# Kernel optimization log

Hardware: AMD Instinct MI355X
Metric: run time of the kernel (lower is better)

The kernel has to match this reference:

```python
import jax, jax.numpy as jnp
import numpy as np

DICT = 32768
TOP_K = 128
LN_EPS = 1e-5


def setup_inputs() -> dict:
    key = jax.random.key(0)
    k_x, k_we, k_be, k_wd, k_bd = jax.random.split(key, 5)
    B, S, D = 4, 2048, 768
    x = jax.random.normal(k_x, (B, S, D), dtype=jnp.float32)
    # nn.Linear stores weight as [out, in]; init scaled roughly like orthogonal gains
    W_enc = jax.random.normal(k_we, (DICT, D), dtype=jnp.float32) / np.sqrt(D)
    b_enc = jax.random.normal(k_be, (DICT,), dtype=jnp.float32) * 0.01
    W_dec = jax.random.normal(k_wd, (D, DICT), dtype=jnp.float32) * (0.1 / np.sqrt(DICT))
    b_dec = jax.random.normal(k_bd, (D,), dtype=jnp.float32) * 0.01
    ln_gamma = jnp.ones((DICT,), dtype=jnp.float32)
    ln_beta = jnp.zeros((DICT,), dtype=jnp.float32)
    return {"x": x, "W_enc": W_enc, "b_enc": b_enc, "ln_gamma": ln_gamma,
            "ln_beta": ln_beta, "W_dec": W_dec, "b_dec": b_dec}


def _layernorm(z, gamma, beta):
    mu = jnp.mean(z, axis=-1, keepdims=True)
    var = jnp.mean(jnp.square(z - mu), axis=-1, keepdims=True)
    return (z - mu) * jax.lax.rsqrt(var + LN_EPS) * gamma + beta


def _top_k_activation(z, k):
    # keep top-k values per row, zero elsewhere (scatter, like torch.scatter_)
    vals, idx = jax.lax.top_k(z, k)            # [B,S,k]
    out = jnp.zeros_like(z)
    return jnp.put_along_axis(out, idx, vals, axis=-1, inplace=False)


def reference(x, W_enc, b_enc, ln_gamma, ln_beta, W_dec, b_dec):
    # encoder: [B,S,D] @ [D,DICT] -> [B,S,DICT]
    z = jnp.einsum("bsd,fd->bsf", x, W_enc) + b_enc
    z = _layernorm(z, ln_gamma, ln_beta)
    z = jax.nn.relu(z)
    features = _top_k_activation(z, TOP_K)      # [B,S,DICT], mostly zero
    output = jnp.einsum("bsf,df->bsd", features, W_dec) + b_dec  # [B,S,D]
    return (output, features)
```

## Files before the change

kernel.cpp:

```cpp
#include <hip/hip_runtime.h>
#include <hip/hip_bf16.h>

#define R_TOT  8192
#define DIM    768
#define FDICT  32768
#define TOPK   128
#define LN_EPS 1e-5f
#define BAND_M 0.12f
#define BAND_CAP 192

using f32x4  = __attribute__((ext_vector_type(4))) float;
using short8 = __attribute__((ext_vector_type(8))) short;

__device__ inline short f2bf(float f) {
    __hip_bfloat16 h = __float2bfloat16(f);
    return *reinterpret_cast<short*>(&h);
}
__device__ inline float bf2f(short s) {
    return __uint_as_float(((unsigned)(unsigned short)s) << 16);
}
__device__ inline void load_lds16(const void* g, void* l) {
    __builtin_amdgcn_global_load_lds(
        (const __attribute__((address_space(1))) unsigned int*)g,
        (__attribute__((address_space(3))) unsigned int*)l, 16, 0, 0);
}

__global__ __launch_bounds__(256) void conv_bf16(
    const float* __restrict__ in, unsigned short* __restrict__ out, int n8)
{
    const int i0 = blockIdx.x * 256 + threadIdx.x;
    const int stride = gridDim.x * 256;
    for (int g = i0; g < n8; g += stride) {
        const float4 a = ((const float4*)in)[g * 2];
        const float4 b = ((const float4*)in)[g * 2 + 1];
        short8 v;
        v[0] = f2bf(a.x); v[1] = f2bf(a.y); v[2] = f2bf(a.z); v[3] = f2bf(a.w);
        v[4] = f2bf(b.x); v[5] = f2bf(b.y); v[6] = f2bf(b.z); v[7] = f2bf(b.w);
        ((short8*)out)[g] = v;
    }
}

#define READ_A(P)                                                              \
    af00 = *(const short8*)&Sb[abase + (2*(P))*1024 + sw0];                    \
    af01 = *(const short8*)&Sb[abase + (2*(P))*1024 + sw1];                    \
    af10 = *(const short8*)&Sb[abase + (2*(P)+1)*1024 + sw0];                  \
    af11 = *(const short8*)&Sb[abase + (2*(P)+1)*1024 + sw1];

#define DO_MFMA(P)                                                             \
    __builtin_amdgcn_s_setprio(1);                                             \
    _Pragma("unroll")                                                          \
    for (int n = 0; n < 4; ++n) {                                              \
        acc[2*(P)][n]   = __builtin_amdgcn_mfma_f32_16x16x32_bf16(af00, bf0[n], acc[2*(P)][n],   0,0,0); \
        acc[2*(P)][n]   = __builtin_amdgcn_mfma_f32_16x16x32_bf16(af01, bf1[n], acc[2*(P)][n],   0,0,0); \
        acc[2*(P)+1][n] = __builtin_amdgcn_mfma_f32_16x16x32_bf16(af10, bf0[n], acc[2*(P)+1][n], 0,0,0); \
        acc[2*(P)+1][n] = __builtin_amdgcn_mfma_f32_16x16x32_bf16(af11, bf1[n], acc[2*(P)+1][n], 0,0,0); \
    }                                                                          \
    __builtin_amdgcn_s_setprio(0);

__global__ __launch_bounds__(512, 2) void enc_gemm(
    const unsigned short* __restrict__ Xb, const unsigned short* __restrict__ Wb,
    const float* __restrict__ benc, unsigned short* __restrict__ Zb)
{
    __shared__ __align__(16) unsigned short S[65536];

    const int t = threadIdx.x;
    const int w = t >> 6, l = t & 63;

    const int cpx = (int)gridDim.x >> 3;
    const int swz = ((int)blockIdx.x & 7) * cpx + ((int)blockIdx.x >> 3);
    const long bm = (long)(swz >> 7) * 256;
    const long bn = (long)(swz & 127) * 256;

    const int wm = w >> 2, wn = w & 3;
    const int lrow = l & 15, l4 = l >> 4;

    const int sw0 = ((l4     ) ^ (lrow & 7)) * 8;
    const int sw1 = ((4 + l4 ) ^ (lrow & 7)) * 8;
    const int abase = wm * 8192 + lrow * 64;
    const int bbase = 16384 + wn * 4096 + lrow * 64;

    const int rh0 = w * 16 + (l >> 3);
    const int rh1 = rh0 + 8;
    const int gsl = ((l & 7) ^ (l >> 3)) * 8;
    const unsigned short* pA00 = Xb + (bm +       rh0) * DIM + gsl;
    const unsigned short* pA01 = Xb + (bm +       rh1) * DIM + gsl;
    const unsigned short* pA10 = Xb + (bm + 128 + rh0) * DIM + gsl;
    const unsigned short* pA11 = Xb + (bm + 128 + rh1) * DIM + gsl;
    const unsigned short* pB00 = Wb + (bn +       rh0) * DIM + gsl;
    const unsigned short* pB01 = Wb + (bn +       rh1) * DIM + gsl;
    const unsigned short* pB10 = Wb + (bn + 128 + rh0) * DIM + gsl;
    const unsigned short* pB11 = Wb + (bn + 128 + rh1) * DIM + gsl;
    const int d00 = w * 1024;
    const int d01 = w * 1024 + 512;

    f32x4 acc[8][4];
#pragma unroll
    for (int m = 0; m < 8; ++m)
#pragma unroll
        for (int n = 0; n < 4; ++n) acc[m][n] = (f32x4){0.f, 0.f, 0.f, 0.f};

    load_lds16(pA00, S + d00);
    load_lds16(pA01, S + d01);
    load_lds16(pA10, S + 8192 + d00);
    load_lds16(pA11, S + 8192 + d01);
    load_lds16(pB00, S + 16384 + d00);
    load_lds16(pB01, S + 16384 + d01);
    load_lds16(pB10, S + 16384 + 8192 + d00);
    load_lds16(pB11, S + 16384 + 8192 + d01);
    pA00 += 64; pA01 += 64; pA10 += 64; pA11 += 64;
    pB00 += 64; pB01 += 64; pB10 += 64; pB11 += 64;

    short8 bf0[4], bf1[4];
    short8 af00, af01, af10, af11;

#pragma unroll 1
    for (int kt = 0; kt < 12; ++kt) {
        const unsigned short* Sb = S + (kt & 1) * 32768;
        unsigned short*       Sn = S + ((kt & 1) ^ 1) * 32768;

        if (kt < 11) {
            load_lds16(pA00, Sn + d00);
            load_lds16(pA01, Sn + d01);
            load_lds16(pA10, Sn + 8192 + d00);
            load_lds16(pA11, Sn + 8192 + d01);
            asm volatile("s_waitcnt vmcnt(4)" ::: "memory");
        } else {
            asm volatile("s_waitcnt vmcnt(0)" ::: "memory");
        }
        __builtin_amdgcn_s_barrier();
#pragma unroll
        for (int n = 0; n < 4; ++n) {
            bf0[n] = *(const short8*)&Sb[bbase + n * 1024 + sw0];
            bf1[n] = *(const short8*)&Sb[bbase + n * 1024 + sw1];
        }
        READ_A(0)
        DO_MFMA(0)
        asm volatile("" ::: "memory");
        __builtin_amdgcn_s_barrier();

        READ_A(1)
        if (kt < 11) {
            load_lds16(pB00, Sn + 16384 + d00);
            load_lds16(pB01, Sn + 16384 + d01);
            load_lds16(pB10, Sn + 16384 + 8192 + d00);
            load_lds16(pB11, Sn + 16384 + 8192 + d01);
        }
        asm volatile("" ::: "memory");
        __builtin_amdgcn_s_barrier();
        DO_MFMA(1)
        asm volatile("" ::: "memory");
        __builtin_amdgcn_s_barrier();

        READ_A(2)
        asm volatile("" ::: "memory");
        __builtin_amdgcn_s_barrier();
        DO_MFMA(2)
        asm volatile("" ::: "memory");
        __builtin_amdgcn_s_barrier();

        READ_A(3)
        asm volatile("" ::: "memory");
        __builtin_amdgcn_s_barrier();
        DO_MFMA(3)
        asm volatile("" ::: "memory");
        __builtin_amdgcn_s_barrier();

        pA00 += 64; pA01 += 64; pA10 += 64; pA11 += 64;
        pB00 += 64; pB01 += 64; pB10 += 64; pB11 += 64;
    }

    __syncthreads();
    float bias[4];
#pragma unroll
    for (int n = 0; n < 4; ++n) bias[n] = benc[bn + wn * 64 + n * 16 + lrow];
    unsigned short* Cs = S;
#pragma unroll
    for (int m = 0; m < 8; ++m)
#pragma unroll
        for (int n = 0; n < 4; ++n)
#pragma unroll
            for (int q = 0; q < 4; ++q)
                Cs[(wm * 128 + m * 16 + l4 * 4 + q) * 256 + wn * 64 + n * 16 + lrow] =
                    (unsigned short)f2bf(acc[m][n][q] + bias[n]);
    __syncthreads();
#pragma unroll
    for (int it = 0; it < 16; ++it) {
        const int g = t + it * 512;
        const int row = g >> 5;
        const int c8 = (g & 31) * 8;
        const short8 v = *(const short8*)&Cs[row * 256 + c8];
        __builtin_nontemporal_store(v, (short8*)&Zb[(bm + row) * FDICT + bn + c8]);
    }
}

__global__ __launch_bounds__(1024) void topk_select(
    const unsigned short* __restrict__ Zb, const float* __restrict__ gamma,
    const float* __restrict__ beta, int* __restrict__ sel_idx,
    float* __restrict__ sel_val, int* __restrict__ band_idx,
    int* __restrict__ cdef, int* __restrict__ nband,
    float* __restrict__ muarr, float* __restrict__ sinvarr)
{
    __shared__ float    redf[32];
    __shared__ int      redi[16];
    __shared__ float    sf[3];
    __shared__ int      stot;
    __shared__ unsigned scomp[2];

    const int t = threadIdx.x;
    const int w = t >> 6;
    const long r = blockIdx.x;

    unsigned u[32];
    float sum = 0.f, sumsq = 0.f;
    const short8* Z8 = (const short8*)(Zb + r * (size_t)FDICT);
#pragma unroll
    for (int q = 0; q < 4; ++q) {
        const short8 v = Z8[q * 1024 + t];
#pragma unroll
        for (int j = 0; j < 8; ++j) {
            const float f = bf2f(v[j]);
            u[q * 8 + j] = __float_as_uint(f);
            sum += f; sumsq += f * f;
        }
    }
#pragma unroll
    for (int o = 32; o > 0; o >>= 1) {
        sum   += __shfl_down(sum, o, 64);
        sumsq += __shfl_down(sumsq, o, 64);
    }
    if ((t & 63) == 0) { redf[w] = sum; redf[16 + w] = sumsq; }
    __syncthreads();
    if (t == 0) {
        float s = 0.f, sq = 0.f;
        for (int i = 0; i < 16; ++i) { s += redf[i]; sq += redf[16 + i]; }
        const float mu = s / (float)FDICT;
        float var = sq / (float)FDICT - mu * mu;
        if (var < 0.f) var = 0.f;
        sf[0] = mu; sf[1] = 1.f / sqrtf(var + LN_EPS);
        scomp[0] = 0; scomp[1] = 0;
    }
    __syncthreads();
    const float mu = sf[0], sinv = sf[1];

    float vmax = 0.f;
#pragma unroll
    for (int q = 0; q < 4; ++q) {
        const size_t base = (size_t)(q * 1024 + t) * 8;
        const float4 g0 = *(const float4*)(gamma + base);
        const float4 g1 = *(const float4*)(gamma + base + 4);
        const float4 b0 = *(const float4*)(beta + base);
        const float4 b1 = *(const float4*)(beta + base + 4);
        const float gs[8] = {g0.x, g0.y, g0.z, g0.w, g1.x, g1.y, g1.z, g1.w};
        const float bs[8] = {b0.x, b0.y, b0.z, b0.w, b1.x, b1.y, b1.z, b1.w};
#pragma unroll
        for (int j = 0; j < 8; ++j) {
            const int i = q * 8 + j;
            const float a = fmaxf(
                fmaf((__uint_as_float(u[i]) - mu) * sinv, gs[j], bs[j]), 0.f);
            u[i] = __float_as_uint(a);
            vmax = fmaxf(vmax, a);
        }
    }
#pragma unroll
    for (int o = 32; o > 0; o >>= 1) vmax = fmaxf(vmax, __shfl_down(vmax, o, 64));
    if ((t & 63) == 0) redf[w] = vmax;
    __syncthreads();
    if (t == 0) {
        float m = 0.f;
        for (int i = 0; i < 16; ++i) m = fmaxf(m, redf[i]);
        sf[2] = m;
    }
    __syncthreads();

    float lo = 0.f, hi = sf[2] + 1e-6f;
#pragma unroll 1
    for (int it = 0; it < 9; ++it) {
        const float thr = 0.5f * (lo + hi);
        int cnt = 0;
#pragma unroll
        for (int i = 0; i < 32; ++i) cnt += (__uint_as_float(u[i]) > thr);
#pragma unroll
        for (int o = 32; o > 0; o >>= 1) cnt += __shfl_down(cnt, o, 64);
        if ((t & 63) == 0) redi[w] = cnt;
        __syncthreads();
        if (t == 0) {
            int s = 0;
            for (int i = 0; i < 16; ++i) s += redi[i];
            stot = s;
        }
        __syncthreads();
        if (stot >= TOPK) lo = thr; else hi = thr;
    }
    const float Tf = 0.5f * (lo + hi);
    const float thi = Tf + BAND_M, tlo = Tf - BAND_M;

#pragma unroll
    for (int i = 0; i < 32; ++i) {
        const float a = __uint_as_float(u[i]);
        const int idx = ((i >> 3) * 1024 + t) * 8 + (i & 7);
        if (a > thi) {
            const unsigned s = atomicAdd(&scomp[0], 1u);
            sel_idx[r * TOPK + s] = idx;
            sel_val[r * TOPK + s] = a;
        } else if (a >= tlo) {
            const unsigned s = atomicAdd(&scomp[1], 1u);
            if (s < BAND_CAP) band_idx[r * BAND_CAP + s] = idx;
        }
    }
    __syncthreads();
    if (t == 0) {
        cdef[r]  = (int)scomp[0];
        int nb = (int)scomp[1]; if (nb > BAND_CAP) nb = BAND_CAP;
        nband[r] = nb;
        muarr[r] = mu; sinvarr[r] = sinv;
    }
}

__global__ __launch_bounds__(256) void refine_select(
    const float* __restrict__ X, const float* __restrict__ Wenc,
    const float* __restrict__ benc, const float* __restrict__ gamma,
    const float* __restrict__ beta, const int* __restrict__ band_idx,
    const int* __restrict__ cdef, const int* __restrict__ nband,
    const float* __restrict__ muarr, const float* __restrict__ sinvarr,
    int* __restrict__ sel_idx, float* __restrict__ sel_val)
{
    __shared__ float xs[DIM];
    __shared__ float cval[BAND_CAP];
    __shared__ int   cidx[BAND_CAP];
    __shared__ int   scnt;
    const int t = threadIdx.x;
    const long r = blockIdx.x;
    const int w = t >> 6, l = t & 63;

    for (int i = t; i < DIM; i += 256) xs[i] = X[r * DIM + i];
    if (t == 0) scnt = 0;
    const int nb = nband[r];
    const int cd = cdef[r];
    int need = TOPK - cd; if (need > nb) need = nb;
    const double mu = (double)muarr[r], sinv = (double)sinvarr[r];
    __syncthreads();

    for (int c = w; c < nb; c += 4) {
        const int fi = band_idx[r * BAND_CAP + c];
        const float* wr = Wenc + (size_t)fi * DIM;
        double s = 0.0;
        for (int k = l; k < DIM; k += 64) s = fma((double)xs[k], (double)wr[k], s);
#pragma unroll
        for (int o = 32; o > 0; o >>= 1) s += __shfl_down(s, o, 64);
        if (l == 0) {
            const double z = s + (double)benc[fi];
            const double a = (z - mu) * sinv * (double)gamma[fi] + (double)beta[fi];
            cval[c] = fmaxf((float)a, 0.f);
            cidx[c] = fi;
        }
    }
    __syncthreads();
    if (t < nb) {
        const float v = cval[t];
        const int id = cidx[t];
        int rank = 0;
        for (int j = 0; j < nb; ++j) {
            const float vj = cval[j];
            rank += (vj > v) || (vj == v && cidx[j] < id);
        }
        if (rank < need) {
            const int s = atomicAdd(&scnt, 1);
            sel_idx[r * TOPK + cd + s] = id;
            sel_val[r * TOPK + cd + s] = v;
        }
    }
}

__global__ __launch_bounds__(256) void transposeWd(
    const float* __restrict__ Wd, unsigned short* __restrict__ WdTb)
{
    __shared__ float tile[32][33];
    const int fx = blockIdx.x * 32;
    const int dy = blockIdx.y * 32;
    const int tx = threadIdx.x & 31;
    const int ty = threadIdx.x >> 5;
    for (int i = ty; i < 32; i += 8)
        tile[i][tx] = Wd[(size_t)(dy + i) * FDICT + fx + tx];
    __syncthreads();
    for (int i = ty; i < 32; i += 8)
        WdTb[(size_t)(fx + i) * DIM + dy + tx] = (unsigned short)f2bf(tile[tx][i]);
}

__global__ __launch_bounds__(384) void decode(
    const int* __restrict__ sel_idx, const float* __restrict__ sel_val,
    const unsigned short* __restrict__ WdTb, const float* __restrict__ bdec,
    float* __restrict__ out)
{
    __shared__ int   sidx[TOPK];
    __shared__ float sval[TOPK];
    const int t = threadIdx.x;
    const long r = blockIdx.x;
    if (t < TOPK) { sidx[t] = sel_idx[r * TOPK + t]; sval[t] = sel_val[r * TOPK + t]; }
    __syncthreads();
    const float2 b2 = *(const float2*)(bdec + t * 2);
    float a0 = b2.x, a1 = b2.y;
    for (int j = 0; j < TOPK; ++j) {
        const unsigned wp = *(const unsigned*)(WdTb + (size_t)sidx[j] * DIM + t * 2);
        const float v = sval[j];
        a0 = fmaf(v, __uint_as_float((wp & 0xFFFFu) << 16), a0);
        a1 = fmaf(v, __uint_as_float(wp & 0xFFFF0000u), a1);
    }
    float2 o2; o2.x = a0; o2.y = a1;
    *(float2*)(out + r * DIM + t * 2) = o2;
}

__global__ __launch_bounds__(1024) void featfill(
    const int* __restrict__ sel_idx, const float* __restrict__ sel_val,
    float* __restrict__ feat)
{
    const int t = threadIdx.x;
    const long r = blockIdx.x;
    const f32x4 z4 = (f32x4){0.f, 0.f, 0.f, 0.f};
    f32x4* row4 = (f32x4*)(feat + r * FDICT);
    for (int i = t; i < FDICT / 4; i += 1024)
        __builtin_nontemporal_store(z4, &row4[i]);
    __syncthreads();
    if (t < TOPK)
        feat[r * FDICT + sel_idx[r * TOPK + t]] = sel_val[r * TOPK + t];
}

extern "C" void kernel_launch(void* const* d_in, const int* in_sizes, int n_in,
                              void* d_out, int out_size, void* d_ws, size_t ws_size,
                              hipStream_t stream)
{
    const float* x     = (const float*)d_in[0];
    const float* Wenc  = (const float*)d_in[1];
    const float* benc  = (const float*)d_in[2];
    const float* gamma = (const float*)d_in[3];
    const float* beta  = (const float*)d_in[4];
    const float* Wdec  = (const float*)d_in[5];
    const float* bdec  = (const float*)d_in[6];

    float* out  = (float*)d_out;
    float* feat = out + (size_t)R_TOT * DIM;

    unsigned short* Xb   = (unsigned short*)out;
    unsigned short* Zb   = (unsigned short*)feat;
    unsigned short* Wb   = (unsigned short*)((char*)feat + 536870912ull);
    unsigned short* WdTb = (unsigned short*)((char*)feat + 587202560ull);

    char* ws = (char*)d_ws;
    int*   sidx  = (int*)ws;
    float* sval  = (float*)(ws + (size_t)R_TOT * TOPK * 4);
    int*   bidx  = (int*)(ws + (size_t)R_TOT * TOPK * 8);
    int*   cdef  = (int*)(ws + (size_t)R_TOT * (TOPK * 8 + BAND_CAP * 4));
    int*   nbnd  = cdef + R_TOT;
    float* muarr = (float*)(nbnd + R_TOT);
    float* sinva = muarr + R_TOT;

    conv_bf16<<<1536, 256, 0, stream>>>(x,    Xb, R_TOT * DIM / 8);
    conv_bf16<<<2048, 256, 0, stream>>>(Wenc, Wb, FDICT * DIM / 8);
    enc_gemm<<<4096, 512, 0, stream>>>(Xb, Wb, benc, Zb);
    topk_select<<<R_TOT, 1024, 0, stream>>>(Zb, gamma, beta, sidx, sval,
                                            bidx, cdef, nbnd, muarr, sinva);
    refine_select<<<R_TOT, 256, 0, stream>>>(x, Wenc, benc, gamma, beta,
                                             bidx, cdef, nbnd, muarr, sinva,
                                             sidx, sval);
    transposeWd<<<dim3(FDICT / 32, DIM / 32), 256, 0, stream>>>(Wdec, WdTb);
    decode<<<R_TOT, 384, 0, stream>>>(sidx, sval, WdTb, bdec, out);
    featfill<<<R_TOT, 1024, 0, stream>>>(sidx, sval, feat);
}
```

Measured before the change: 2.041 ms.

## Fuse feature zero-fill and scatter into select kernels when workspace is large

When the workspace holds at least 624 MiB, the bf16 Z, W_enc and transposed W_dec buffers move there instead of aliasing the features output. topk_select then zero-fills its feature row and scatters the confident picks, refine_select scatters the band picks, and the separate featfill launch is dropped. The per-block reductions also stop using a thread-0 serial reduce plus an extra barrier: every thread sums the partials from LDS, and the bisection loop double-buffers its counts. This works only if the workspace is large enough; otherwise it falls back to the old path.

```diff
diff --git a/kernel.cpp b/kernel.cpp
--- a/kernel.cpp
+++ b/kernel.cpp
@@ -198,12 +198,12 @@
     const float* __restrict__ beta, int* __restrict__ sel_idx,
     float* __restrict__ sel_val, int* __restrict__ band_idx,
     int* __restrict__ cdef, int* __restrict__ nband,
-    float* __restrict__ muarr, float* __restrict__ sinvarr)
+    float* __restrict__ muarr, float* __restrict__ sinvarr,
+    float* __restrict__ feat)
 {
     __shared__ float    redf[32];
-    __shared__ int      redi[16];
-    __shared__ float    sf[3];
-    __shared__ int      stot;
+    __shared__ float    redm[16];
+    __shared__ int      redi[2][16];
     __shared__ unsigned scomp[2];
 
     const int t = threadIdx.x;
@@ -223,6 +223,16 @@
             sum += f; sumsq += f * f;
         }
     }
+    if (t == 0) { scomp[0] = 0; scomp[1] = 0; }
+
+    if (feat) {
+        const f32x4 z4 = (f32x4){0.f, 0.f, 0.f, 0.f};
+        f32x4* row4 = (f32x4*)(feat + r * (size_t)FDICT);
+#pragma unroll
+        for (int q = 0; q < 8; ++q)
+            __builtin_nontemporal_store(z4, &row4[q * 1024 + t]);
+    }
+
 #pragma unroll
     for (int o = 32; o > 0; o >>= 1) {
         sum   += __shfl_down(sum, o, 64);
@@ -230,17 +240,13 @@
     }
     if ((t & 63) == 0) { redf[w] = sum; redf[16 + w] = sumsq; }
     __syncthreads();
-    if (t == 0) {
-        float s = 0.f, sq = 0.f;
-        for (int i = 0; i < 16; ++i) { s += redf[i]; sq += redf[16 + i]; }
-        const float mu = s / (float)FDICT;
-        float var = sq / (float)FDICT - mu * mu;
-        if (var < 0.f) var = 0.f;
-        sf[0] = mu; sf[1] = 1.f / sqrtf(var + LN_EPS);
-        scomp[0] = 0; scomp[1] = 0;
-    }
-    __syncthreads();
-    const float mu = sf[0], sinv = sf[1];
+    float s_ = 0.f, sq_ = 0.f;
+#pragma unroll
+    for (int i = 0; i < 16; ++i) { s_ += redf[i]; sq_ += redf[16 + i]; }
+    const float mu = s_ / (float)FDICT;
+    float var = sq_ / (float)FDICT - mu * mu;
+    if (var < 0.f) var = 0.f;
+    const float sinv = 1.f / sqrtf(var + LN_EPS);
 
     float vmax = 0.f;
 #pragma unroll
@@ -263,16 +269,13 @@
     }
 #pragma unroll
     for (int o = 32; o > 0; o >>= 1) vmax = fmaxf(vmax, __shfl_down(vmax, o, 64));
-    if ((t & 63) == 0) redf[w] = vmax;
-    __syncthreads();
-    if (t == 0) {
-        float m = 0.f;
-        for (int i = 0; i < 16; ++i) m = fmaxf(m, redf[i]);
-        sf[2] = m;
-    }
-    __syncthreads();
-
-    float lo = 0.f, hi = sf[2] + 1e-6f;
+    if ((t & 63) == 0) redm[w] = vmax;
+    __syncthreads();
+    float m_ = 0.f;
+#pragma unroll
+    for (int i = 0; i < 16; ++i) m_ = fmaxf(m_, redm[i]);
+
+    float lo = 0.f, hi = m_ + 1e-6f;
 #pragma unroll 1
     for (int it = 0; it < 9; ++it) {
         const float thr = 0.5f * (lo + hi);
@@ -281,14 +284,11 @@
         for (int i = 0; i < 32; ++i) cnt += (__uint_as_float(u[i]) > thr);
 #pragma unroll
         for (int o = 32; o > 0; o >>= 1) cnt += __shfl_down(cnt, o, 64);
-        if ((t & 63) == 0) redi[w] = cnt;
+        if ((t & 63) == 0) redi[it & 1][w] = cnt;
         __syncthreads();
-        if (t == 0) {
-            int s = 0;
-            for (int i = 0; i < 16; ++i) s += redi[i];
-            stot = s;
-        }
-        __syncthreads();
+        int stot = 0;
+#pragma unroll
+        for (int i = 0; i < 16; ++i) stot += redi[it & 1][i];
         if (stot >= TOPK) lo = thr; else hi = thr;
     }
     const float Tf = 0.5f * (lo + hi);
@@ -302,6 +302,7 @@
             const unsigned s = atomicAdd(&scomp[0], 1u);
             sel_idx[r * TOPK + s] = idx;
             sel_val[r * TOPK + s] = a;
+            if (feat) feat[r * (size_t)FDICT + idx] = a;
         } else if (a >= tlo) {
             const unsigned s = atomicAdd(&scomp[1], 1u);
             if (s < BAND_CAP) band_idx[r * BAND_CAP + s] = idx;
@@ -322,7 +323,8 @@
     const float* __restrict__ beta, const int* __restrict__ band_idx,
     const int* __restrict__ cdef, const int* __restrict__ nband,
     const float* __restrict__ muarr, const float* __restrict__ sinvarr,
-    int* __restrict__ sel_idx, float* __restrict__ sel_val)
+    int* __restrict__ sel_idx, float* __restrict__ sel_val,
+    float* __restrict__ feat)
 {
     __shared__ float xs[DIM];
     __shared__ float cval[BAND_CAP];
@@ -367,6 +369,7 @@
             const int s = atomicAdd(&scnt, 1);
             sel_idx[r * TOPK + cd + s] = id;
             sel_val[r * TOPK + cd + s] = v;
+            if (feat) feat[r * (size_t)FDICT + id] = v;
         }
     }
 }
@@ -439,10 +442,7 @@
     float* out  = (float*)d_out;
     float* feat = out + (size_t)R_TOT * DIM;
 
-    unsigned short* Xb   = (unsigned short*)out;
-    unsigned short* Zb   = (unsigned short*)feat;
-    unsigned short* Wb   = (unsigned short*)((char*)feat + 536870912ull);
-    unsigned short* WdTb = (unsigned short*)((char*)feat + 587202560ull);
+    unsigned short* Xb = (unsigned short*)out;
 
     char* ws = (char*)d_ws;
     int*   sidx  = (int*)ws;
@@ -453,15 +453,32 @@
     float* muarr = (float*)(nbnd + R_TOT);
     float* sinva = muarr + R_TOT;
 
+    const size_t WS_NEED = 624ull << 20;
+    const bool big = (ws_size >= WS_NEED);
+
+    unsigned short* Zb, *Wb, *WdTb;
+    if (big) {
+        Zb   = (unsigned short*)(ws + (16ull << 20));
+        Wb   = (unsigned short*)(ws + (528ull << 20));
+        WdTb = (unsigned short*)(ws + (576ull << 20));
+    } else {
+        Zb   = (unsigned short*)feat;
+        Wb   = (unsigned short*)((char*)feat + 536870912ull);
+        WdTb = (unsigned short*)((char*)feat + 587202560ull);
+    }
+    float* featArg = big ? feat : nullptr;
+
     conv_bf16<<<1536, 256, 0, stream>>>(x,    Xb, R_TOT * DIM / 8);
     conv_bf16<<<2048, 256, 0, stream>>>(Wenc, Wb, FDICT * DIM / 8);
     enc_gemm<<<4096, 512, 0, stream>>>(Xb, Wb, benc, Zb);
     topk_select<<<R_TOT, 1024, 0, stream>>>(Zb, gamma, beta, sidx, sval,
-                                            bidx, cdef, nbnd, muarr, sinva);
+                                            bidx, cdef, nbnd, muarr, sinva,
+                                            featArg);
     refine_select<<<R_TOT, 256, 0, stream>>>(x, Wenc, benc, gamma, beta,
                                              bidx, cdef, nbnd, muarr, sinva,
-                                             sidx, sval);
+                                             sidx, sval, featArg);
     transposeWd<<<dim3(FDICT / 32, DIM / 32), 256, 0, stream>>>(Wdec, WdTb);
     decode<<<R_TOT, 384, 0, stream>>>(sidx, sval, WdTb, bdec, out);
-    featfill<<<R_TOT, 1024, 0, stream>>>(sidx, sval, feat);
-}
+    if (!big)
+        featfill<<<R_TOT, 1024, 0, stream>>>(sidx, sval, feat);
+}
```

Measured after the change: 1.915 ms. 6.2% less time.
